# Kernel tuning notes

Hardware: AMD Instinct MI355X
Metric: run time of the kernel (lower is better)

## Reference

```python
import jax, jax.numpy as jnp
import numpy as np
import math

N_HEAD = 16
HEAD_DIM = 64
N_EMBD = N_HEAD * HEAD_DIM  # 1024


def _alibi_slopes(n_heads):
    def pow2(n):
        start = 2.0 ** (-2.0 ** (-(math.log2(n) - 3)))
        return [start * (start ** i) for i in range(n)]
    if n_heads & (n_heads - 1) == 0:
        s = pow2(n_heads)
    else:
        cp2 = 2 ** math.floor(math.log2(n_heads))
        s = pow2(cp2)
        extra_base = 2.0 ** (-2.0 ** (-(math.log2(2 * cp2) - 3)))
        s += [extra_base * (extra_base ** i) for i in range(n_heads - cp2)]
        s = s[:n_heads]
    return jnp.asarray(np.array(s, dtype=np.float32))


def setup_inputs() -> dict:
    key = jax.random.key(0)
    k1, k2, k3, k4 = jax.random.split(key, 4)
    B, T = 2, 2048
    x = jax.random.normal(k1, (B, T, N_EMBD), dtype=jnp.float32)
    # c_attn weight for q,k (use_v=True -> 2*n_embd outputs), no bias
    W_attn = jax.random.normal(k2, (N_EMBD, 2 * N_EMBD), dtype=jnp.float32) * 0.02
    v_tmp = jax.random.normal(k3, (N_HEAD, N_HEAD), dtype=jnp.float32) * 0.02
    proj_tmp = jax.random.normal(k4, (N_HEAD, N_HEAD), dtype=jnp.float32) * 0.02
    return {"x": x, "W_attn": W_attn, "v_tmp": v_tmp, "proj_tmp": proj_tmp}


def reference(x, W_attn, v_tmp, proj_tmp):
    B, T, C = x.shape
    H, D = N_HEAD, HEAD_DIM
    scale = 1.0 / math.sqrt(D)

    qk = x @ W_attn  # (B,T,2C)
    q, k = qk[..., :C], qk[..., C:]
    q = q.reshape(B, T, H, D).transpose(0, 2, 1, 3)  # (B,H,T,D)
    k = k.reshape(B, T, H, D).transpose(0, 2, 1, 3)

    # V via Kronecker-lifted matrix: x @ kron(v_tmp, I_D)
    # block structure => mix head channels: out[...,j,d] = sum_i x[...,i,d]*v_tmp[i,j]
    xh = x.reshape(B, T, H, D)
    v = jnp.einsum('btid,ij->btjd', xh, v_tmp)  # (B,T,H,D)

    scores = jnp.einsum('bhqd,bhkd->bhqk', q, k) * scale  # (B,H,T,T)

    # ALiBi bias + causal mask
    pos = jnp.arange(T, dtype=jnp.float32)
    rel = pos[None, :] - pos[:, None]  # (T,T), mem - ctx
    slopes = _alibi_slopes(H)
    bias = slopes[:, None, None] * rel[None, :, :]
    causal = pos[None, :] <= pos[:, None]
    bias = jnp.where(causal[None, :, :], bias, -jnp.inf)
    scores = scores + bias[None]

    att = jax.nn.softmax(scores, axis=-1)
    y = jnp.einsum('bhqk,bkhd->bqhd', att, v)  # (B,T,H,D)

    # output proj via kron(proj_tmp, I_D).T: out[...,i,d] = sum_j y[...,j,d]*proj_tmp[i,j]
    y = jnp.einsum('btjd,ij->btid', y, proj_tmp)
    return y.reshape(B, T, C)
```

## Files before the change

kernel.cpp:

```cpp
#include <hip/hip_runtime.h>

typedef __attribute__((ext_vector_type(8))) __bf16 bf16x8;
typedef __attribute__((ext_vector_type(8))) unsigned short u16x8;
typedef __attribute__((ext_vector_type(4))) float f32x4;
typedef __attribute__((ext_vector_type(4))) unsigned int u32x4;

#define LOG2E 1.4426950408889634f

#define GLDS16(gp, lp)                                                \
  __builtin_amdgcn_global_load_lds(                                   \
      (const __attribute__((address_space(1))) void*)(gp),            \
      (__attribute__((address_space(3))) void*)(lp), 16, 0, 0)

__device__ __forceinline__ unsigned short f2b(float f) {
  return __builtin_bit_cast(unsigned short, (__bf16)f);
}
__device__ __forceinline__ float b2f(unsigned short h) {
  return __uint_as_float(((unsigned)h) << 16);
}
__device__ __forceinline__ unsigned cvt_pk(float a, float b) {
  unsigned r;
  asm("v_cvt_pk_bf16_f32 %0, %1, %2" : "=v"(r) : "v"(a), "v"(b));
  return r;
}
__device__ __forceinline__ void swap32(unsigned& a, unsigned& b) {
  asm("v_permlane32_swap_b32 %0, %1" : "+v"(a), "+v"(b));
}
__device__ __forceinline__ void swap16(unsigned& a, unsigned& b) {
  asm("v_permlane16_swap_b32 %0, %1" : "+v"(a), "+v"(b));
}

__global__ __launch_bounds__(256) void k_pre(const float* __restrict__ x,
                                             const float* __restrict__ vt,
                                             const float* __restrict__ W,
                                             unsigned short* __restrict__ xb,
                                             unsigned short* __restrict__ vb,
                                             unsigned short* __restrict__ Wt) {
  if (blockIdx.x < 1024) {
    __shared__ float s_vt[256];
    s_vt[threadIdx.x] = vt[threadIdx.x];
    __syncthreads();
    int g = blockIdx.x * 256 + threadIdx.x;
    int bt = g >> 6, d = g & 63;
    const float* xp = x + (size_t)bt * 1024 + d;
    float xi[16];
#pragma unroll
    for (int i = 0; i < 16; ++i) xi[i] = xp[i * 64];
#pragma unroll
    for (int i = 0; i < 16; ++i) xb[(size_t)bt * 1024 + i * 64 + d] = f2b(xi[i]);
#pragma unroll
    for (int j = 0; j < 16; ++j) {
      float s = 0.f;
#pragma unroll
      for (int i = 0; i < 16; ++i) s += xi[i] * s_vt[i * 16 + j];
      vb[(size_t)bt * 1024 + j * 64 + d] = f2b(s);
    }
  } else {
    __shared__ unsigned short tile[64][65];
    int id2 = blockIdx.x - 1024;
    int n0 = (id2 & 31) * 64;
    int k0 = (id2 >> 5) * 64;
    int tx = threadIdx.x & 63, ty = threadIdx.x >> 6;
#pragma unroll
    for (int r = 0; r < 16; ++r) {
      int kk = ty * 16 + r;
      tile[kk][tx] = f2b(W[(size_t)(k0 + kk) * 2048 + n0 + tx]);
    }
    __syncthreads();
#pragma unroll
    for (int r = 0; r < 16; ++r) {
      int nn = ty * 16 + r;
      Wt[(size_t)(n0 + nn) * 1024 + k0 + tx] = tile[tx][nn];
    }
  }
}

__global__ __launch_bounds__(256) void k_mid(const unsigned short* __restrict__ A,
                                             const unsigned short* __restrict__ Bt,
                                             unsigned short* __restrict__ C,
                                             const unsigned short* __restrict__ vb,
                                             unsigned short* __restrict__ Vt) {
  if (blockIdx.x < 512) {
    __shared__ unsigned short As[128 * 32];
    __shared__ unsigned short Bs[128 * 32];
    const int K = 1024;
    int m0 = (blockIdx.x & 31) * 128;
    int n0 = (blockIdx.x >> 5) * 128;
    int tid = threadIdx.x;
    int w = tid >> 6, lane = tid & 63;
    int lq = lane & 15, lk8 = (lane >> 4) * 8;
    int wr = (w >> 1) * 64, wc = (w & 1) * 64;
    f32x4 acc[4][4];
#pragma unroll
    for (int i = 0; i < 4; ++i)
#pragma unroll
      for (int j = 0; j < 4; ++j)
#pragma unroll
        for (int r = 0; r < 4; ++r) acc[i][j][r] = 0.f;

    for (int kk = 0; kk < K; kk += 32) {
      __syncthreads();
#pragma unroll
      for (int i = 0; i < 2; ++i) {
        int c = tid + 256 * i;
        int row = c >> 2, col = (c & 3) * 8;
        GLDS16(A + (size_t)(m0 + row) * K + kk + col, As + c * 8);
        GLDS16(Bt + (size_t)(n0 + row) * K + kk + col, Bs + c * 8);
      }
      __syncthreads();
      bf16x8 af[4], bf[4];
#pragma unroll
      for (int i = 0; i < 4; ++i) af[i] = *(const bf16x8*)(As + (wr + i * 16 + lq) * 32 + lk8);
#pragma unroll
      for (int j = 0; j < 4; ++j) bf[j] = *(const bf16x8*)(Bs + (wc + j * 16 + lq) * 32 + lk8);
#pragma unroll
      for (int i = 0; i < 4; ++i)
#pragma unroll
        for (int j = 0; j < 4; ++j)
          acc[i][j] = __builtin_amdgcn_mfma_f32_16x16x32_bf16(af[i], bf[j], acc[i][j], 0, 0, 0);
    }
#pragma unroll
    for (int i = 0; i < 4; ++i)
#pragma unroll
      for (int j = 0; j < 4; ++j)
#pragma unroll
        for (int r = 0; r < 4; ++r) {
          int m = m0 + wr + i * 16 + (lane >> 4) * 4 + r;
          int n = n0 + wc + j * 16 + lq;
          C[(size_t)m * 2048 + n] = f2b(acc[i][j][r]);
        }
  } else {
    __shared__ unsigned short tile[64][65];
    int id2 = blockIdx.x - 512;
    int t0 = (id2 & 31) * 64;
    int c0 = ((id2 >> 5) & 15) * 64;
    int b = id2 >> 9;
    int tx = threadIdx.x & 63, ty = threadIdx.x >> 6;
#pragma unroll
    for (int r = 0; r < 16; ++r) {
      int tt = ty * 16 + r;
      tile[tt][tx] = vb[((size_t)b * 2048 + t0 + tt) * 1024 + c0 + tx];
    }
    __syncthreads();
#pragma unroll
    for (int r = 0; r < 16; ++r) {
      int cc = ty * 16 + r;
      Vt[((size_t)b * 1024 + c0 + cc) * 2048 + t0 + tx] = tile[tx][cc];
    }
  }
}

__global__ __launch_bounds__(256, 4) void k_flash(const unsigned short* __restrict__ qkb,
                                                  const unsigned short* __restrict__ Vt,
                                                  unsigned short* __restrict__ y) {
  __shared__ unsigned short Ks[3][2][64 * 32];
  __shared__ unsigned short Vs[3][2][64 * 32];
  int id = blockIdx.x;
  int xcd = id & 7, s = id >> 3;
  int grp = xcd + 8 * (s & 3);
  int qt = 31 - (s >> 2);
  int hd = grp & 15, b = grp >> 4;
  int tid = threadIdx.x;
  int w = tid >> 6, lane = tid & 63;
  int quad = lane >> 4, lq = lane & 15, lk8 = quad * 8;
  int xk8 = (quad ^ ((lq >> 1) & 3)) * 8;
  int qh = w >> 1, kh = w & 1;
  int rs = tid >> 2;
  int csw = ((tid & 3) ^ ((tid >> 3) & 3)) * 8;
  int ld = rs * 32 + (tid & 3) * 8;
  const size_t rowb = (size_t)b * 2048;
  const size_t vrow = ((size_t)b * 1024 + hd * 64 + rs) * 2048 + csw;
  const size_t krow = ((rowb + rs) << 11) + 1024 + hd * 64 + csw;

  float slope = exp2f(-0.5f * (float)(hd + 1));
  const float c1 = 0.125f * LOG2E;
  const float c2 = slope * LOG2E;
  const float c16 = 16.0f * c2;
  const float SHIFT = 16.0f;

  bf16x8 ones;
#pragma unroll
  for (int i = 0; i < 8; ++i) ones[i] = (__bf16)1.0f;

  int q0 = qt * 64;
  int qrow = q0 + qh * 32;
  bf16x8 qf[2][2];
#pragma unroll
  for (int qs2 = 0; qs2 < 2; ++qs2) {
    int qg = qrow + qs2 * 16 + lq;
    qf[qs2][0] = *(const bf16x8*)(qkb + ((rowb + qg) << 11) + hd * 64 + lk8);
    qf[qs2][1] = *(const bf16x8*)(qkb + ((rowb + qg) << 11) + hd * 64 + 32 + lk8);
  }
  int kq0 = kh * 32 + quad * 4 - qrow - lq;
  float base0[4];
#pragma unroll
  for (int r = 0; r < 4; ++r) base0[r] = c2 * (float)(kq0 + r) - SHIFT;

  f32x4 o[4][2];
  f32x4 o4[2];
#pragma unroll
  for (int r = 0; r < 4; ++r) { o4[0][r] = 0.f; o4[1][r] = 0.f; }
#pragma unroll
  for (int jj = 0; jj < 4; ++jj)
#pragma unroll
    for (int qs2 = 0; qs2 < 2; ++qs2)
#pragma unroll
      for (int r = 0; r < 4; ++r) o[jj][qs2][r] = 0.f;

  GLDS16(qkb + krow,      &Ks[0][0][ld]);
  GLDS16(qkb + krow + 32, &Ks[0][1][ld]);
  GLDS16(Vt + vrow,       &Vs[0][0][ld]);
  GLDS16(Vt + vrow + 32,  &Vs[0][1][ld]);
  if (qt >= 1) {
    size_t koff = 64;
    GLDS16(qkb + krow + (koff << 11),      &Ks[1][0][ld]);
    GLDS16(qkb + krow + (koff << 11) + 32, &Ks[1][1][ld]);
    GLDS16(Vt + vrow + koff,               &Vs[1][0][ld]);
    GLDS16(Vt + vrow + koff + 32,          &Vs[1][1][ld]);
    asm volatile("s_waitcnt vmcnt(4)" ::: "memory");
  } else {
    asm volatile("s_waitcnt vmcnt(0)" ::: "memory");
  }
  __builtin_amdgcn_s_barrier();
  __builtin_amdgcn_sched_barrier(0);
  int cur = 0;

#pragma unroll 1
  for (int kt = 0; kt <= qt; ++kt) {
    int k0 = kt * 64;
    if (kt + 2 <= qt) {
      int c2i = cur + 2; if (c2i >= 3) c2i -= 3;
      size_t koff = (size_t)(k0 + 128);
      GLDS16(qkb + krow + (koff << 11),      &Ks[c2i][0][ld]);
      GLDS16(qkb + krow + (koff << 11) + 32, &Ks[c2i][1][ld]);
      GLDS16(Vt + vrow + koff,               &Vs[c2i][0][ld]);
      GLDS16(Vt + vrow + koff + 32,          &Vs[c2i][1][ld]);
    }
    bf16x8 kc[2][2];
#pragma unroll
    for (int ks2 = 0; ks2 < 2; ++ks2) {
      u16x8 t0 = *(const u16x8*)(&Ks[cur][0][(kh * 32 + ks2 * 16 + lq) * 32 + xk8]);
      u16x8 t1 = *(const u16x8*)(&Ks[cur][1][(kh * 32 + ks2 * 16 + lq) * 32 + xk8]);
      kc[ks2][0] = __builtin_bit_cast(bf16x8, t0);
      kc[ks2][1] = __builtin_bit_cast(bf16x8, t1);
    }
    __builtin_amdgcn_s_setprio(1);
    f32x4 S[2][2];
#pragma unroll
    for (int ks2 = 0; ks2 < 2; ++ks2)
#pragma unroll
      for (int qs2 = 0; qs2 < 2; ++qs2) {
        f32x4 a;
#pragma unroll
        for (int r = 0; r < 4; ++r) a[r] = 0.f;
        a = __builtin_amdgcn_mfma_f32_16x16x32_bf16(kc[ks2][0], qf[qs2][0], a, 0, 0, 0);
        a = __builtin_amdgcn_mfma_f32_16x16x32_bf16(kc[ks2][1], qf[qs2][1], a, 0, 0, 0);
        S[ks2][qs2] = a;
      }
    __builtin_amdgcn_s_setprio(0);
    float bk = c2 * (float)k0;
    float p[2][2][4];
    if (kt == qt) {
#pragma unroll
      for (int ks2 = 0; ks2 < 2; ++ks2)
#pragma unroll
        for (int qs2 = 0; qs2 < 2; ++qs2)
#pragma unroll
          for (int r = 0; r < 4; ++r) {
            float v = S[ks2][qs2][r] * c1 + (base0[r] + bk + c16 * (float)(ks2 - qs2));
            v = (k0 + kq0 + (ks2 - qs2) * 16 + r <= 0) ? v : -1e30f;
            p[ks2][qs2][r] = exp2f(v);
          }
    } else {
#pragma unroll
      for (int ks2 = 0; ks2 < 2; ++ks2)
#pragma unroll
        for (int qs2 = 0; qs2 < 2; ++qs2)
#pragma unroll
          for (int r = 0; r < 4; ++r) {
            float v = S[ks2][qs2][r] * c1 + (base0[r] + bk + c16 * (float)(ks2 - qs2));
            p[ks2][qs2][r] = exp2f(v);
          }
    }
    unsigned pk[2][2][2];
#pragma unroll
    for (int ks2 = 0; ks2 < 2; ++ks2)
#pragma unroll
      for (int qs2 = 0; qs2 < 2; ++qs2) {
        pk[ks2][qs2][0] = cvt_pk(p[ks2][qs2][0], p[ks2][qs2][1]);
        pk[ks2][qs2][1] = cvt_pk(p[ks2][qs2][2], p[ks2][qs2][3]);
      }
    bf16x8 pf[2];
#pragma unroll
    for (int qs2 = 0; qs2 < 2; ++qs2) {
      unsigned a0 = pk[0][qs2][0], b0 = pk[1][qs2][0];
      swap32(a0, b0); swap16(a0, b0);
      unsigned a1 = pk[0][qs2][1], b1 = pk[1][qs2][1];
      swap32(a1, b1); swap16(a1, b1);
      u32x4 t; t[0] = a0; t[1] = a1; t[2] = b0; t[3] = b1;
      pf[qs2] = __builtin_bit_cast(bf16x8, t);
    }
    __builtin_amdgcn_s_setprio(1);
    o4[0] = __builtin_amdgcn_mfma_f32_16x16x32_bf16(ones, pf[0], o4[0], 0, 0, 0);
    o4[1] = __builtin_amdgcn_mfma_f32_16x16x32_bf16(ones, pf[1], o4[1], 0, 0, 0);
#pragma unroll
    for (int jj = 0; jj < 4; ++jj) {
      u16x8 v0 = *(const u16x8*)(&Vs[cur][kh][(jj * 16 + lq) * 32 + xk8]);
      bf16x8 vf = __builtin_bit_cast(bf16x8, v0);
      o[jj][0] = __builtin_amdgcn_mfma_f32_16x16x32_bf16(vf, pf[0], o[jj][0], 0, 0, 0);
      o[jj][1] = __builtin_amdgcn_mfma_f32_16x16x32_bf16(vf, pf[1], o[jj][1], 0, 0, 0);
    }
    __builtin_amdgcn_s_setprio(0);
    if (kt < qt) {
      if (kt + 2 <= qt) asm volatile("s_waitcnt vmcnt(4)" ::: "memory");
      else              asm volatile("s_waitcnt vmcnt(0)" ::: "memory");
      __builtin_amdgcn_s_barrier();
      __builtin_amdgcn_sched_barrier(0);
      ++cur; if (cur == 3) cur = 0;
    }
  }

  __syncthreads();
  float* red0 = (float*)&Ks[0][0][0];
  float* red1 = (float*)&Vs[0][0][0];
  float* red = (qh ? red1 : red0) + lane * 36;
  if (kh == 1) {
#pragma unroll
    for (int jj = 0; jj < 4; ++jj)
#pragma unroll
      for (int qs2 = 0; qs2 < 2; ++qs2)
#pragma unroll
        for (int r = 0; r < 4; ++r) red[(jj * 2 + qs2) * 4 + r] = o[jj][qs2][r];
    red[32] = o4[0][0];
    red[33] = o4[1][0];
  }
  __syncthreads();
  if (kh == 0) {
#pragma unroll
    for (int jj = 0; jj < 4; ++jj)
#pragma unroll
      for (int qs2 = 0; qs2 < 2; ++qs2)
#pragma unroll
        for (int r = 0; r < 4; ++r) o[jj][qs2][r] += red[(jj * 2 + qs2) * 4 + r];
    float inv0 = 1.0f / (o4[0][0] + red[32]);
    float inv1 = 1.0f / (o4[1][0] + red[33]);
#pragma unroll
    for (int qs2 = 0; qs2 < 2; ++qs2) {
      float inv = qs2 ? inv1 : inv0;
      size_t base = ((rowb + qrow + qs2 * 16 + lq) << 10) + hd * 64 + quad * 4;
#pragma unroll
      for (int jj = 0; jj < 4; ++jj) {
        ushort4 pk4;
        pk4.x = f2b(o[jj][qs2][0] * inv);
        pk4.y = f2b(o[jj][qs2][1] * inv);
        pk4.z = f2b(o[jj][qs2][2] * inv);
        pk4.w = f2b(o[jj][qs2][3] * inv);
        *(ushort4*)(y + base + jj * 16) = pk4;
      }
    }
  }
}

__global__ __launch_bounds__(256) void k_proj(const unsigned short* __restrict__ yb,
                                              const float* __restrict__ pt,
                                              float* __restrict__ out) {
  __shared__ float s_pt[256];
  s_pt[threadIdx.x] = pt[threadIdx.x];
  __syncthreads();
  int g = blockIdx.x * 256 + threadIdx.x;
  int bt = g >> 6, d = g & 63;
  float yj[16];
#pragma unroll
  for (int j = 0; j < 16; ++j) yj[j] = b2f(yb[(size_t)bt * 1024 + j * 64 + d]);
#pragma unroll
  for (int i = 0; i < 16; ++i) {
    float s = 0.f;
#pragma unroll
    for (int j = 0; j < 16; ++j) s += yj[j] * s_pt[i * 16 + j];
    out[(size_t)bt * 1024 + i * 64 + d] = s;
  }
}

extern "C" void kernel_launch(void* const* d_in, const int* in_sizes, int n_in,
                              void* d_out, int out_size, void* d_ws, size_t ws_size,
                              hipStream_t stream) {
  const float* x  = (const float*)d_in[0];
  const float* W  = (const float*)d_in[1];
  const float* vt = (const float*)d_in[2];
  const float* pt = (const float*)d_in[3];
  float* out = (float*)d_out;

  char* ws = (char*)d_ws;
  unsigned short* xb  = (unsigned short*)(ws);
  unsigned short* Wt  = (unsigned short*)(ws + (8u  << 20));
  unsigned short* qkb = (unsigned short*)(ws + (12u << 20));
  unsigned short* vb  = (unsigned short*)(ws + (28u << 20));
  unsigned short* Vtr = (unsigned short*)(ws + (36u << 20));
  unsigned short* yb  = xb;

  k_pre  <<<1536, 256, 0, stream>>>(x, vt, W, xb, vb, Wt);
  k_mid  <<<1536, 256, 0, stream>>>(xb, Wt, qkb, vb, Vtr);
  k_flash<<<1024, 256, 0, stream>>>(qkb, Vtr, yb);
  k_proj <<<1024, 256, 0, stream>>>(yb, pt, out);
}
```

Baseline: 151.9 us.

## Widen flash blocks to 128 query rows with 8 warps sharing K/V tiles

The flash kernel now launches 512-thread blocks that each handle 128 query rows (four query groups by two key halves) instead of 64. Each K/V tile loaded into LDS is reused by twice as many warps, and each thread issues half as many async loads per tile. Query-block scheduling is reordered to pair long and short causal blocks so the load stays balanced. The trade-offs are fewer blocks (512), a lower occupancy bound, and a masking check that now runs per warp on diagonal tiles.

```diff
diff --git a/kernel.cpp b/kernel.cpp
--- a/kernel.cpp
+++ b/kernel.cpp
@@ -150,27 +150,30 @@
   }
 }
 
-__global__ __launch_bounds__(256, 4) void k_flash(const unsigned short* __restrict__ qkb,
+__global__ __launch_bounds__(512, 2) void k_flash(const unsigned short* __restrict__ qkb,
                                                   const unsigned short* __restrict__ Vt,
                                                   unsigned short* __restrict__ y) {
   __shared__ unsigned short Ks[3][2][64 * 32];
   __shared__ unsigned short Vs[3][2][64 * 32];
   int id = blockIdx.x;
-  int xcd = id & 7, s = id >> 3;
-  int grp = xcd + 8 * (s & 3);
-  int qt = 31 - (s >> 2);
+  int xcd = id & 7, u = id >> 3;
+  int grp = xcd + 8 * (u & 3);
+  int v = u >> 2;
+  int qblk = (v < 8) ? (15 - v) : (v - 8);
   int hd = grp & 15, b = grp >> 4;
   int tid = threadIdx.x;
   int w = tid >> 6, lane = tid & 63;
   int quad = lane >> 4, lq = lane & 15, lk8 = quad * 8;
   int xk8 = (quad ^ ((lq >> 1) & 3)) * 8;
-  int qh = w >> 1, kh = w & 1;
-  int rs = tid >> 2;
-  int csw = ((tid & 3) ^ ((tid >> 3) & 3)) * 8;
-  int ld = rs * 32 + (tid & 3) * 8;
+  int qg = w >> 1, kh = w & 1;
+  int half = tid >> 8;
+  int cc = tid & 255;
+  int rs = cc >> 2, chunk = cc & 3;
+  int csw = (chunk ^ ((cc >> 3) & 3)) * 8;
+  int ld = rs * 32 + chunk * 8;
   const size_t rowb = (size_t)b * 2048;
-  const size_t vrow = ((size_t)b * 1024 + hd * 64 + rs) * 2048 + csw;
-  const size_t krow = ((rowb + rs) << 11) + 1024 + hd * 64 + csw;
+  const size_t vrow = ((size_t)b * 1024 + hd * 64 + rs) * 2048 + half * 32 + csw;
+  const size_t krow = ((rowb + rs) << 11) + 1024 + hd * 64 + half * 32 + csw;
 
   float slope = exp2f(-0.5f * (float)(hd + 1));
   const float c1 = 0.125f * LOG2E;
@@ -182,14 +185,15 @@
 #pragma unroll
   for (int i = 0; i < 8; ++i) ones[i] = (__bf16)1.0f;
 
-  int q0 = qt * 64;
-  int qrow = q0 + qh * 32;
+  int q0 = qblk * 128;
+  int qrow = q0 + qg * 32;
+  const int ktlast = 2 * qblk + 1;
   bf16x8 qf[2][2];
 #pragma unroll
   for (int qs2 = 0; qs2 < 2; ++qs2) {
-    int qg = qrow + qs2 * 16 + lq;
-    qf[qs2][0] = *(const bf16x8*)(qkb + ((rowb + qg) << 11) + hd * 64 + lk8);
-    qf[qs2][1] = *(const bf16x8*)(qkb + ((rowb + qg) << 11) + hd * 64 + 32 + lk8);
+    int qgl = qrow + qs2 * 16 + lq;
+    qf[qs2][0] = *(const bf16x8*)(qkb + ((rowb + qgl) << 11) + hd * 64 + lk8);
+    qf[qs2][1] = *(const bf16x8*)(qkb + ((rowb + qgl) << 11) + hd * 64 + 32 + lk8);
   }
   int kq0 = kh * 32 + quad * 4 - qrow - lq;
   float base0[4];
@@ -207,34 +211,26 @@
 #pragma unroll
       for (int r = 0; r < 4; ++r) o[jj][qs2][r] = 0.f;
 
-  GLDS16(qkb + krow,      &Ks[0][0][ld]);
-  GLDS16(qkb + krow + 32, &Ks[0][1][ld]);
-  GLDS16(Vt + vrow,       &Vs[0][0][ld]);
-  GLDS16(Vt + vrow + 32,  &Vs[0][1][ld]);
-  if (qt >= 1) {
+  GLDS16(qkb + krow, &Ks[0][half][ld]);
+  GLDS16(Vt + vrow,  &Vs[0][half][ld]);
+  {
     size_t koff = 64;
-    GLDS16(qkb + krow + (koff << 11),      &Ks[1][0][ld]);
-    GLDS16(qkb + krow + (koff << 11) + 32, &Ks[1][1][ld]);
-    GLDS16(Vt + vrow + koff,               &Vs[1][0][ld]);
-    GLDS16(Vt + vrow + koff + 32,          &Vs[1][1][ld]);
-    asm volatile("s_waitcnt vmcnt(4)" ::: "memory");
-  } else {
-    asm volatile("s_waitcnt vmcnt(0)" ::: "memory");
+    GLDS16(qkb + krow + (koff << 11), &Ks[1][half][ld]);
+    GLDS16(Vt + vrow + koff,          &Vs[1][half][ld]);
+    asm volatile("s_waitcnt vmcnt(2)" ::: "memory");
   }
   __builtin_amdgcn_s_barrier();
   __builtin_amdgcn_sched_barrier(0);
   int cur = 0;
 
 #pragma unroll 1
-  for (int kt = 0; kt <= qt; ++kt) {
+  for (int kt = 0; kt <= ktlast; ++kt) {
     int k0 = kt * 64;
-    if (kt + 2 <= qt) {
+    if (kt + 2 <= ktlast) {
       int c2i = cur + 2; if (c2i >= 3) c2i -= 3;
       size_t koff = (size_t)(k0 + 128);
-      GLDS16(qkb + krow + (koff << 11),      &Ks[c2i][0][ld]);
-      GLDS16(qkb + krow + (koff << 11) + 32, &Ks[c2i][1][ld]);
-      GLDS16(Vt + vrow + koff,               &Vs[c2i][0][ld]);
-      GLDS16(Vt + vrow + koff + 32,          &Vs[c2i][1][ld]);
+      GLDS16(qkb + krow + (koff << 11), &Ks[c2i][half][ld]);
+      GLDS16(Vt + vrow + koff,          &Vs[c2i][half][ld]);
     }
     bf16x8 kc[2][2];
 #pragma unroll
@@ -260,16 +256,16 @@
     __builtin_amdgcn_s_setprio(0);
     float bk = c2 * (float)k0;
     float p[2][2][4];
-    if (kt == qt) {
+    if (k0 + 64 > qrow) {
 #pragma unroll
       for (int ks2 = 0; ks2 < 2; ++ks2)
 #pragma unroll
         for (int qs2 = 0; qs2 < 2; ++qs2)
 #pragma unroll
           for (int r = 0; r < 4; ++r) {
-            float v = S[ks2][qs2][r] * c1 + (base0[r] + bk + c16 * (float)(ks2 - qs2));
-            v = (k0 + kq0 + (ks2 - qs2) * 16 + r <= 0) ? v : -1e30f;
-            p[ks2][qs2][r] = exp2f(v);
+            float vv = S[ks2][qs2][r] * c1 + (base0[r] + bk + c16 * (float)(ks2 - qs2));
+            vv = (k0 + kq0 + (ks2 - qs2) * 16 + r <= 0) ? vv : -1e30f;
+            p[ks2][qs2][r] = exp2f(vv);
           }
     } else {
 #pragma unroll
@@ -278,8 +274,8 @@
         for (int qs2 = 0; qs2 < 2; ++qs2)
 #pragma unroll
           for (int r = 0; r < 4; ++r) {
-            float v = S[ks2][qs2][r] * c1 + (base0[r] + bk + c16 * (float)(ks2 - qs2));
-            p[ks2][qs2][r] = exp2f(v);
+            float vv = S[ks2][qs2][r] * c1 + (base0[r] + bk + c16 * (float)(ks2 - qs2));
+            p[ks2][qs2][r] = exp2f(vv);
           }
     }
     unsigned pk[2][2][2];
@@ -311,9 +307,9 @@
       o[jj][1] = __builtin_amdgcn_mfma_f32_16x16x32_bf16(vf, pf[1], o[jj][1], 0, 0, 0);
     }
     __builtin_amdgcn_s_setprio(0);
-    if (kt < qt) {
-      if (kt + 2 <= qt) asm volatile("s_waitcnt vmcnt(4)" ::: "memory");
-      else              asm volatile("s_waitcnt vmcnt(0)" ::: "memory");
+    if (kt < ktlast) {
+      if (kt + 2 <= ktlast) asm volatile("s_waitcnt vmcnt(2)" ::: "memory");
+      else                  asm volatile("s_waitcnt vmcnt(0)" ::: "memory");
       __builtin_amdgcn_s_barrier();
       __builtin_amdgcn_sched_barrier(0);
       ++cur; if (cur == 3) cur = 0;
@@ -321,9 +317,8 @@
   }
 
   __syncthreads();
-  float* red0 = (float*)&Ks[0][0][0];
-  float* red1 = (float*)&Vs[0][0][0];
-  float* red = (qh ? red1 : red0) + lane * 36;
+  float* red = (qg < 2 ? (float*)&Ks[0][0][0] + (qg * 64 + lane) * 36
+                       : (float*)&Vs[0][0][0] + ((qg - 2) * 64 + lane) * 36);
   if (kh == 1) {
 #pragma unroll
     for (int jj = 0; jj < 4; ++jj)
@@ -400,6 +395,6 @@
 
   k_pre  <<<1536, 256, 0, stream>>>(x, vt, W, xb, vb, Wt);
   k_mid  <<<1536, 256, 0, stream>>>(xb, Wt, qkb, vb, Vtr);
-  k_flash<<<1024, 256, 0, stream>>>(qkb, Vtr, yb);
+  k_flash<<<512, 512, 0, stream>>>(qkb, Vtr, yb);
   k_proj <<<1024, 256, 0, stream>>>(yb, pt, out);
 }
```

After: 157.6 us. 3.7% more time.
